# Kernel optimization log

Measured on AMD Instinct MI355X. Metric: run time of the kernel, lower is better.

## Reference

```python
import jax, jax.numpy as jnp
from jax import lax
import numpy as np

B = 128          # batch size
S = 207          # input spatial size implied by outputSpatialSize=[8,8]
N_PTS = 256000
NEG = -1e30      # -inf stand-in for masked max-pooling
# BNReLU channel counts in execution order: 8 resnet blocks x (bn1, bn2), final resnet BN(32), last BN(64)
SIZES = [8,8,8,8,8,16,16,16,16,24,24,24,24,32,32,32,32,64]
OFF = np.cumsum([0] + SIZES)

WSHAPES = dict(conv0=(3,3,1,8),
               c1a=(3,3,8,8), c1b=(3,3,8,8), c2a=(3,3,8,8), c2b=(3,3,8,8),
               c3a=(3,3,8,16), c3b=(3,3,16,16), c3r=(3,3,8,16),
               c4a=(3,3,16,16), c4b=(3,3,16,16),
               c5a=(3,3,16,24), c5b=(3,3,24,24), c5r=(3,3,16,24),
               c6a=(3,3,24,24), c6b=(3,3,24,24),
               c7a=(3,3,24,32), c7b=(3,3,32,32), c7r=(3,3,24,32),
               c8a=(3,3,32,32), c8b=(3,3,32,32),
               conv_last=(5,5,32,64))

def _conv(x, w, stride, padding):
    return lax.conv_general_dilated(x, w, (stride, stride), padding,
                                    dimension_numbers=('NHWC', 'HWIO', 'NHWC'))

def _pool_max(x, win, stride, init):
    return lax.reduce_window(x, init, lax.max, (1, win, win, 1), (1, stride, stride, 1), 'VALID')

def _bnrelu(x, m, g, b):
    # eval-mode BN folded to affine, applied on active sites only (inactive stay exactly 0)
    return m * jax.nn.relu(x * g + b)

def _subconv(x, w, m):
    # submanifold conv == dense conv on zero-filled grid, output restricted to active sites
    return _conv(x, w, 1, 'SAME') * m

def _strided(x, w, m, win, stride):
    # scn.Convolution: output site active iff any active input in its receptive field
    m2 = _pool_max(m, win, stride, 0.0)
    return _conv(x, w, stride, 'VALID') * m2, m2

def _block(x, m, g1, b1, w1, g2, b2, w2, wres, stride):
    # pre-activation basic block from scn.SparseResNet
    h = _bnrelu(x, m, g1, b1)
    if stride == 1:
        h, m2 = _subconv(h, w1, m), m
    else:
        h, m2 = _strided(h, w1, m, 3, 2)
    h = _subconv(_bnrelu(h, m2, g2, b2), w2, m2)
    r = x if wres is None else _strided(x, wres, m, 3, 2)[0]
    return h + r, m2

def _forward(locations, batch_idx, features, bn_gamma, bn_beta, W):
    idx = (batch_idx, locations[:, 0], locations[:, 1], jnp.zeros_like(batch_idx))
    x = jnp.zeros((B, S, S, 1), jnp.float32).at[idx].add(features[:, 0])  # InputLayer (sum dups)
    m = jnp.zeros((B, S, S, 1), jnp.float32).at[idx].set(1.0)             # active-site mask
    g = [bn_gamma[OFF[i]:OFF[i+1]] for i in range(len(SIZES))]
    b = [bn_beta[OFF[i]:OFF[i+1]] for i in range(len(SIZES))]
    x = _subconv(x, W['conv0'], m)                              # 1->8 @ 207x207
    # MaxPooling(pool 3, stride 2) over active sites only
    m2 = _pool_max(m, 3, 2, 0.0)
    x = jnp.where(m2 > 0, _pool_max(jnp.where(m > 0, x, NEG), 3, 2, NEG), 0.0)
    m = m2                                                      # @ 103x103
    blocks = [('c1a', 'c1b', None, 1), ('c2a', 'c2b', None, 1),
              ('c3a', 'c3b', 'c3r', 2), ('c4a', 'c4b', None, 1),
              ('c5a', 'c5b', 'c5r', 2), ('c6a', 'c6b', None, 1),
              ('c7a', 'c7b', 'c7r', 2), ('c8a', 'c8b', None, 1)]
    for i, (k1, k2, kr, st) in enumerate(blocks):
        x, m = _block(x, m, g[2*i], b[2*i], W[k1], g[2*i+1], b[2*i+1], W[k2],
                      None if kr is None else W[kr], st)        # 103->51->25->12
    x = _bnrelu(x, m, g[16], b[16])                             # final resnet BNReLU(32)
    x, m = _strided(x, W['conv_last'], m, 5, 1)                 # 32->64, 12x12 -> 8x8
    x = _bnrelu(x, m, g[17], b[17])
    flat = x.transpose(0, 3, 1, 2).reshape(B, -1)               # SparseToDense + flatten (NCHW order)
    return (flat @ W['w_lin'].T).reshape(B, -1, 1)              # [B, 100, 1]

def setup_inputs():
    key = jax.random.key(0)
    ks = iter(jax.random.split(key, 64))
    inp = {
        'locations': jax.random.randint(next(ks), (N_PTS, 2), 0, S, dtype=jnp.int32),
        'batch_idx': jax.random.randint(next(ks), (N_PTS,), 0, B, dtype=jnp.int32),
        'features': jax.random.normal(next(ks), (N_PTS, 1), jnp.float32),
        'bn_gamma': 1.0 + 0.1 * jax.random.normal(next(ks), (int(OFF[-1]),), jnp.float32),
        'bn_beta': 0.1 * jax.random.normal(next(ks), (int(OFF[-1]),), jnp.float32),
    }
    for name, shp in WSHAPES.items():
        fan_in = int(np.prod(shp[:-1]))
        inp[name] = jax.random.normal(next(ks), shp, jnp.float32) * (2.0 / fan_in) ** 0.5
    inp['w_lin'] = jax.random.normal(next(ks), (100, 64 * 8 * 8), jnp.float32) * (1.0 / 4096.0) ** 0.5
    return inp

def reference(locations, batch_idx, features, bn_gamma, bn_beta, conv0,
              c1a, c1b, c2a, c2b, c3a, c3b, c3r, c4a, c4b, c5a, c5b, c5r,
              c6a, c6b, c7a, c7b, c7r, c8a, c8b, conv_last, w_lin):
    W = dict(conv0=conv0, c1a=c1a, c1b=c1b, c2a=c2a, c2b=c2b, c3a=c3a, c3b=c3b, c3r=c3r,
             c4a=c4a, c4b=c4b, c5a=c5a, c5b=c5b, c5r=c5r, c6a=c6a, c6b=c6b,
             c7a=c7a, c7b=c7b, c7r=c7r, c8a=c8a, c8b=c8b, conv_last=conv_last, w_lin=w_lin)
    return _forward(locations, batch_idx, features, bn_gamma, bn_beta, W)
```

## Files before the change

kernel.cpp:

```cpp
#include <hip/hip_runtime.h>

#define S 207
#define BATCH 128
#define NPTS 256000

static const int OFFS[19] = {0,8,16,24,32,40,56,72,88,104,128,152,176,200,232,264,296,328,392};

__global__ void zero2_kernel(float4* __restrict__ a, float4* __restrict__ b, int n4) {
    int i = blockIdx.x * blockDim.x + threadIdx.x;
    if (i < n4) { a[i] = make_float4(0,0,0,0); b[i] = make_float4(0,0,0,0); }
}

__global__ void zero_kernel(float* __restrict__ p, int n) {
    int i = blockIdx.x * blockDim.x + threadIdx.x;
    if (i < n) p[i] = 0.0f;
}

__global__ void scatter_kernel(const int* __restrict__ loc, const int* __restrict__ bidx,
                               const float* __restrict__ feat,
                               float* __restrict__ xs, float* __restrict__ ms) {
    int t = blockIdx.x * blockDim.x + threadIdx.x;
    if (t >= NPTS) return;
    int b = bidx[t];
    int r = loc[2 * t];
    int c = loc[2 * t + 1];
    int idx = (b * S + r) * S + c;
    atomicAdd(&xs[idx], feat[t]);
    ms[idx] = 1.0f;
}

__global__ __launch_bounds__(256) void conv0_pool_kernel(
    const float* __restrict__ xs, const float* __restrict__ ms,
    const float* __restrict__ w,
    float* __restrict__ x1, float* __restrict__ m1) {
    const int Hout = 103;
    int opix = blockIdx.x * 256 + threadIdx.x;
    int total = BATCH * Hout * Hout;
    if (opix >= total) return;
    int wo = opix % Hout;
    int t = opix / Hout;
    int ho = t % Hout;
    int b  = t / Hout;

    float mv[3][3];
    float mwin = 0.0f;
    #pragma unroll
    for (int pi = 0; pi < 3; ++pi)
        #pragma unroll
        for (int pj = 0; pj < 3; ++pj) {
            float m = ms[(b * S + 2 * ho + pi) * S + 2 * wo + pj];
            mv[pi][pj] = m;
            mwin = fmaxf(mwin, m);
        }
    float* xp = x1 + (size_t)opix * 8;
    if (mwin <= 0.0f) {
        *(float4*)xp = make_float4(0,0,0,0);
        *(float4*)(xp + 4) = make_float4(0,0,0,0);
        m1[opix] = 0.0f;
        return;
    }
    float p[5][5];
    #pragma unroll
    for (int r = 0; r < 5; ++r) {
        int ii = 2 * ho - 1 + r;
        #pragma unroll
        for (int c = 0; c < 5; ++c) {
            int jj = 2 * wo - 1 + c;
            bool ok = ((unsigned)ii < (unsigned)S) && ((unsigned)jj < (unsigned)S);
            p[r][c] = ok ? xs[(b * S + ii) * S + jj] : 0.0f;
        }
    }
    float best[8];
    #pragma unroll
    for (int co = 0; co < 8; ++co) best[co] = -1e30f;
    #pragma unroll
    for (int pi = 0; pi < 3; ++pi)
        #pragma unroll
        for (int pj = 0; pj < 3; ++pj) {
            if (mv[pi][pj] > 0.0f) {
                float acc[8];
                #pragma unroll
                for (int co = 0; co < 8; ++co) acc[co] = 0.0f;
                #pragma unroll
                for (int kh = 0; kh < 3; ++kh)
                    #pragma unroll
                    for (int kw = 0; kw < 3; ++kw) {
                        float x = p[pi + kh][pj + kw];
                        #pragma unroll
                        for (int co = 0; co < 8; ++co)
                            acc[co] = fmaf(x, w[(kh * 3 + kw) * 8 + co], acc[co]);
                    }
                #pragma unroll
                for (int co = 0; co < 8; ++co) best[co] = fmaxf(best[co], acc[co]);
            }
        }
    *(float4*)xp = make_float4(best[0], best[1], best[2], best[3]);
    *(float4*)(xp + 4) = make_float4(best[4], best[5], best[6], best[7]);
    m1[opix] = 1.0f;
}

template <int K, int CIN, int COUT, int COT, bool BN, bool RES>
__global__ __launch_bounds__(256) void fconv_kernel(
    const float* __restrict__ in, const float* __restrict__ w,
    const float* __restrict__ g, const float* __restrict__ bbn,
    const float* __restrict__ mIn, const float* __restrict__ mOut,
    const float* __restrict__ res, float* __restrict__ out,
    int Hin, int Hout, int stride, int pad) {
    const int Win = Hin, Wout = Hout;
    int npix = BATCH * Hout * Wout;
    int opix = blockIdx.x * 256 + threadIdx.x;
    if (opix >= npix) return;
    int co0 = blockIdx.y * COT;
    int wo = opix % Wout;
    int t = opix / Wout;
    int ho = t % Hout;
    int b  = t / Hout;

    float mo = mOut[opix];
    float* op = out + (size_t)opix * COUT + co0;
    if (mo <= 0.0f) {
        #pragma unroll
        for (int j = 0; j < COT; j += 4) {
            float4 r4 = RES ? *(const float4*)(res + (size_t)opix * COUT + co0 + j)
                            : make_float4(0,0,0,0);
            *(float4*)(op + j) = r4;
        }
        return;
    }
    float acc[COT];
    #pragma unroll
    for (int j = 0; j < COT; ++j) acc[j] = 0.0f;

    #pragma unroll
    for (int kh = 0; kh < K; ++kh) {
        int ih = ho * stride + kh - pad;
        if ((unsigned)ih >= (unsigned)Hin) continue;
        #pragma unroll
        for (int kw = 0; kw < K; ++kw) {
            int iw = wo * stride + kw - pad;
            if ((unsigned)iw >= (unsigned)Win) continue;
            int ipix = (b * Hin + ih) * Win + iw;
            float mi = 1.0f;
            if (BN) { mi = mIn[ipix]; if (mi <= 0.0f) continue; }
            const float* ip = in + (size_t)ipix * CIN;
            const float* wp = w + (kh * K + kw) * CIN * COUT + co0;
            #pragma unroll
            for (int ci = 0; ci < CIN; ci += 4) {
                float4 xv = *(const float4*)(ip + ci);
                if (BN) {
                    xv.x = mi * fmaxf(fmaf(xv.x, g[ci],     bbn[ci]),     0.0f);
                    xv.y = mi * fmaxf(fmaf(xv.y, g[ci + 1], bbn[ci + 1]), 0.0f);
                    xv.z = mi * fmaxf(fmaf(xv.z, g[ci + 2], bbn[ci + 2]), 0.0f);
                    xv.w = mi * fmaxf(fmaf(xv.w, g[ci + 3], bbn[ci + 3]), 0.0f);
                }
                #pragma unroll
                for (int j = 0; j < COT; ++j) {
                    acc[j] = fmaf(xv.x, wp[(ci    ) * COUT + j], acc[j]);
                    acc[j] = fmaf(xv.y, wp[(ci + 1) * COUT + j], acc[j]);
                    acc[j] = fmaf(xv.z, wp[(ci + 2) * COUT + j], acc[j]);
                    acc[j] = fmaf(xv.w, wp[(ci + 3) * COUT + j], acc[j]);
                }
            }
        }
    }
    #pragma unroll
    for (int j = 0; j < COT; j += 4) {
        float4 o4;
        o4.x = acc[j] * mo; o4.y = acc[j+1] * mo; o4.z = acc[j+2] * mo; o4.w = acc[j+3] * mo;
        if (RES) {
            float4 r4 = *(const float4*)(res + (size_t)opix * COUT + co0 + j);
            o4.x += r4.x; o4.y += r4.y; o4.z += r4.z; o4.w += r4.w;
        }
        *(float4*)(op + j) = o4;
    }
}

template <int CIN, int COUT, int COT>
__global__ __launch_bounds__(256) void strided_ra_kernel(
    const float* __restrict__ in,
    const float* __restrict__ wR, const float* __restrict__ wA,
    const float* __restrict__ g, const float* __restrict__ bbn,
    const float* __restrict__ mIn, float* __restrict__ mOutBuf,
    float* __restrict__ outR, float* __restrict__ outA,
    int Hin, int Hout) {
    constexpr int NG = COUT / COT;
    int npix = BATCH * Hout * Hout;
    int opix = blockIdx.x * 256 + threadIdx.x;
    if (opix >= npix) return;
    int path = blockIdx.y / NG;
    int co0  = (blockIdx.y % NG) * COT;
    int wo = opix % Hout;
    int t = opix / Hout;
    int ho = t % Hout;
    int b  = t / Hout;

    const float* wsel = path ? wA : wR;
    float acc[COT];
    #pragma unroll
    for (int j = 0; j < COT; ++j) acc[j] = 0.0f;
    float m2 = 0.0f;

    #pragma unroll
    for (int kh = 0; kh < 3; ++kh) {
        int ih = 2 * ho + kh;
        #pragma unroll
        for (int kw = 0; kw < 3; ++kw) {
            int iw = 2 * wo + kw;
            int ipix = (b * Hin + ih) * Hin + iw;
            float mi = mIn[ipix];
            if (mi <= 0.0f) continue;
            m2 = fmaxf(m2, mi);
            const float* ip = in + (size_t)ipix * CIN;
            const float* wp = wsel + (kh * 3 + kw) * CIN * COUT + co0;
            #pragma unroll
            for (int ci = 0; ci < CIN; ci += 4) {
                float4 xv = *(const float4*)(ip + ci);
                if (path) {
                    xv.x = mi * fmaxf(fmaf(xv.x, g[ci],     bbn[ci]),     0.0f);
                    xv.y = mi * fmaxf(fmaf(xv.y, g[ci + 1], bbn[ci + 1]), 0.0f);
                    xv.z = mi * fmaxf(fmaf(xv.z, g[ci + 2], bbn[ci + 2]), 0.0f);
                    xv.w = mi * fmaxf(fmaf(xv.w, g[ci + 3], bbn[ci + 3]), 0.0f);
                }
                #pragma unroll
                for (int j = 0; j < COT; ++j) {
                    acc[j] = fmaf(xv.x, wp[(ci    ) * COUT + j], acc[j]);
                    acc[j] = fmaf(xv.y, wp[(ci + 1) * COUT + j], acc[j]);
                    acc[j] = fmaf(xv.z, wp[(ci + 2) * COUT + j], acc[j]);
                    acc[j] = fmaf(xv.w, wp[(ci + 3) * COUT + j], acc[j]);
                }
            }
        }
    }
    if (blockIdx.y == 0) mOutBuf[opix] = m2;
    float* op = (path ? outA : outR) + (size_t)opix * COUT + co0;
    #pragma unroll
    for (int j = 0; j < COT; j += 4) {
        float4 o4;
        o4.x = acc[j] * m2; o4.y = acc[j+1] * m2; o4.z = acc[j+2] * m2; o4.w = acc[j+3] * m2;
        *(float4*)(op + j) = o4;
    }
}

__global__ void pool_kernel(const float* __restrict__ in, float* __restrict__ out,
                            int Hin, int Win, int Hout, int Wout, int win, int stride) {
    int tid = blockIdx.x * blockDim.x + threadIdx.x;
    int total = BATCH * Hout * Wout;
    if (tid >= total) return;
    int wo = tid % Wout;
    int p = tid / Wout;
    int ho = p % Hout;
    int b  = p / Hout;
    float mx = 0.0f;
    for (int i = 0; i < win; ++i)
        for (int j = 0; j < win; ++j)
            mx = fmaxf(mx, in[(b * Hin + ho * stride + i) * Win + wo * stride + j]);
    out[tid] = mx;
}

__global__ __launch_bounds__(256) void bn_tr_kernel(
    const float* __restrict__ x, const float* __restrict__ m,
    const float* __restrict__ g, const float* __restrict__ bb,
    float* __restrict__ xt) {
    int tid = blockIdx.x * 256 + threadIdx.x;
    if (tid >= BATCH * 4096) return;
    int c = tid & 63, hw = (tid >> 6) & 63, b = tid >> 12;
    float v = m[b * 64 + hw] * fmaxf(fmaf(x[tid], g[c], bb[c]), 0.0f);
    xt[((size_t)b << 12) + c * 64 + hw] = v;
}

__global__ __launch_bounds__(256) void linear_gemm_kernel(
    const float* __restrict__ xt, const float* __restrict__ wl,
    float* __restrict__ out) {
    int o = blockIdx.x;
    int half = threadIdx.x >> 7;
    int b = threadIdx.x & 127;
    int k0 = blockIdx.y * 512 + half * 256;
    const float* xp = xt + ((size_t)b << 12) + k0;
    const float* wp = wl + o * 4096 + k0;
    float acc = 0.0f;
    #pragma unroll 16
    for (int k = 0; k < 256; k += 4) {
        float4 xv = *(const float4*)(xp + k);
        float4 wv = *(const float4*)(wp + k);
        acc = fmaf(xv.x, wv.x, acc); acc = fmaf(xv.y, wv.y, acc);
        acc = fmaf(xv.z, wv.z, acc); acc = fmaf(xv.w, wv.w, acc);
    }
    atomicAdd(&out[b * 100 + o], acc);
}

template <int K, int CIN, int COUT, int COT, bool BN, bool RES>
static inline void fconv(hipStream_t s, const float* in, const float* w,
                         const float* g, const float* bbn,
                         const float* mIn, const float* mOut, const float* res,
                         float* out, int Hin, int Hout, int stride, int pad) {
    int npix = BATCH * Hout * Hout;
    dim3 grid((npix + 255) / 256, COUT / COT);
    fconv_kernel<K, CIN, COUT, COT, BN, RES><<<grid, 256, 0, s>>>(
        in, w, g, bbn, mIn, mOut, res, out, Hin, Hout, stride, pad);
}

template <int CIN, int COUT, int COT>
static inline void strided_ra(hipStream_t s, const float* in, const float* wR, const float* wA,
                              const float* g, const float* bbn, const float* mIn,
                              float* mOutBuf, float* outR, float* outA, int Hin, int Hout) {
    int npix = BATCH * Hout * Hout;
    dim3 grid((npix + 255) / 256, 2 * (COUT / COT));
    strided_ra_kernel<CIN, COUT, COT><<<grid, 256, 0, s>>>(
        in, wR, wA, g, bbn, mIn, mOutBuf, outR, outA, Hin, Hout);
}

extern "C" void kernel_launch(void* const* d_in, const int* in_sizes, int n_in,
                              void* d_out, int out_size, void* d_ws, size_t ws_size,
                              hipStream_t stream) {
    const int*   loc   = (const int*)d_in[0];
    const int*   bidx  = (const int*)d_in[1];
    const float* feat  = (const float*)d_in[2];
    const float* gamma = (const float*)d_in[3];
    const float* beta  = (const float*)d_in[4];
    const float* Wconv0 = (const float*)d_in[5];
    const float* Wc1a = (const float*)d_in[6];
    const float* Wc1b = (const float*)d_in[7];
    const float* Wc2a = (const float*)d_in[8];
    const float* Wc2b = (const float*)d_in[9];
    const float* Wc3a = (const float*)d_in[10];
    const float* Wc3b = (const float*)d_in[11];
    const float* Wc3r = (const float*)d_in[12];
    const float* Wc4a = (const float*)d_in[13];
    const float* Wc4b = (const float*)d_in[14];
    const float* Wc5a = (const float*)d_in[15];
    const float* Wc5b = (const float*)d_in[16];
    const float* Wc5r = (const float*)d_in[17];
    const float* Wc6a = (const float*)d_in[18];
    const float* Wc6b = (const float*)d_in[19];
    const float* Wc7a = (const float*)d_in[20];
    const float* Wc7b = (const float*)d_in[21];
    const float* Wc7r = (const float*)d_in[22];
    const float* Wc8a = (const float*)d_in[23];
    const float* Wc8b = (const float*)d_in[24];
    const float* Wlast = (const float*)d_in[25];
    const float* wlin  = (const float*)d_in[26];

    const size_t SZB = (size_t)BATCH * 103 * 103 * 8;
    const size_t SZM = (size_t)BATCH * 103 * 103;
    float* b0 = (float*)d_ws;
    float* b1 = b0 + SZB;
    float* b2 = b1 + SZB;
    float* m0 = b2 + SZB;
    float* m1 = m0 + SZM;

    const float* G[18];
    const float* Bt[18];
    for (int i = 0; i < 18; ++i) { G[i] = gamma + OFFS[i]; Bt[i] = beta + OFFS[i]; }

    {
        int n = BATCH * S * S;
        zero2_kernel<<<(n / 4 + 255) / 256, 256, 0, stream>>>((float4*)b1, (float4*)b2, n / 4);
        scatter_kernel<<<(NPTS + 255) / 256, 256, 0, stream>>>(loc, bidx, feat, b1, b2);
        int total = BATCH * 103 * 103;
        conv0_pool_kernel<<<(total + 255) / 256, 256, 0, stream>>>(b1, b2, Wconv0, b0, m0);
    }

    fconv<3, 8, 8, 8, true, false>(stream, b0, Wc1a, G[0], Bt[0], m0, m0, nullptr, b1, 103, 103, 1, 1);
    fconv<3, 8, 8, 8, true, true >(stream, b1, Wc1b, G[1], Bt[1], m0, m0, b0,      b2, 103, 103, 1, 1);
    fconv<3, 8, 8, 8, true, false>(stream, b2, Wc2a, G[2], Bt[2], m0, m0, nullptr, b0, 103, 103, 1, 1);
    fconv<3, 8, 8, 8, true, true >(stream, b0, Wc2b, G[3], Bt[3], m0, m0, b2,      b1, 103, 103, 1, 1);
    strided_ra<8, 16, 8>(stream, b1, Wc3r, Wc3a, G[4], Bt[4], m0, m1, b0, b2, 103, 51);
    fconv<3, 16, 16, 8, true, true >(stream, b2, Wc3b, G[5], Bt[5], m1, m1, b0, b1, 51, 51, 1, 1);
    fconv<3, 16, 16, 8, true, false>(stream, b1, Wc4a, G[6], Bt[6], m1, m1, nullptr, b0, 51, 51, 1, 1);
    fconv<3, 16, 16, 8, true, true >(stream, b0, Wc4b, G[7], Bt[7], m1, m1, b1,      b2, 51, 51, 1, 1);
    strided_ra<16, 24, 8>(stream, b2, Wc5r, Wc5a, G[8], Bt[8], m1, m0, b0, b1, 51, 25);
    fconv<3, 24, 24, 8, true, true >(stream, b1, Wc5b, G[9], Bt[9], m0, m0, b0, b2, 25, 25, 1, 1);
    fconv<3, 24, 24, 8, true, false>(stream, b2, Wc6a, G[10], Bt[10], m0, m0, nullptr, b0, 25, 25, 1, 1);
    fconv<3, 24, 24, 8, true, true >(stream, b0, Wc6b, G[11], Bt[11], m0, m0, b2,      b1, 25, 25, 1, 1);
    strided_ra<24, 32, 4>(stream, b1, Wc7r, Wc7a, G[12], Bt[12], m0, m1, b0, b2, 25, 12);
    fconv<3, 32, 32, 4, true, true >(stream, b2, Wc7b, G[13], Bt[13], m1, m1, b0, b1, 12, 12, 1, 1);
    fconv<3, 32, 32, 4, true, false>(stream, b1, Wc8a, G[14], Bt[14], m1, m1, nullptr, b0, 12, 12, 1, 1);
    fconv<3, 32, 32, 4, true, true >(stream, b0, Wc8b, G[15], Bt[15], m1, m1, b1,      b2, 12, 12, 1, 1);
    pool_kernel<<<(BATCH * 64 + 255) / 256, 256, 0, stream>>>(m1, m0, 12, 12, 8, 8, 5, 1);
    fconv<5, 32, 64, 4, true, false>(stream, b2, Wlast, G[16], Bt[16], m1, m0, nullptr, b0, 12, 8, 1, 0);
    bn_tr_kernel<<<(BATCH * 4096 + 255) / 256, 256, 0, stream>>>(b0, m0, G[17], Bt[17], b1);
    zero_kernel<<<(BATCH * 100 + 255) / 256, 256, 0, stream>>>((float*)d_out, BATCH * 100);
    linear_gemm_kernel<<<dim3(100, 8), 256, 0, stream>>>(b1, wlin, (float*)d_out);
}
```

Measured before the change: 907.9 us.

## Fuse first two 8-channel resnet blocks into tiled shared-memory kernel

Adds a resblock kernel that fuses BN-ReLU, two 3x3 submanifold convs and the residual add for one block. It stages a halo tile of the input in shared memory and keeps the intermediate activation on chip, and it is used for the two 103x103 blocks. This removes two full-resolution global round trips per block and two launches, at the cost of recomputing halo pixels. The COT template argument of the strided_ra calls also changes, and buffers are reassigned to fit the new chain.

```diff
diff --git a/kernel.cpp b/kernel.cpp
--- a/kernel.cpp
+++ b/kernel.cpp
@@ -97,6 +97,118 @@
     *(float4*)xp = make_float4(best[0], best[1], best[2], best[3]);
     *(float4*)(xp + 4) = make_float4(best[4], best[5], best[6], best[7]);
     m1[opix] = 1.0f;
+}
+
+template <int C, int TILE, int NTX>
+__global__ __launch_bounds__(256) void resblock_kernel(
+    const float* __restrict__ in, const float* __restrict__ mask,
+    const float* __restrict__ w1, const float* __restrict__ w2,
+    const float* __restrict__ g1, const float* __restrict__ bb1,
+    const float* __restrict__ g2, const float* __restrict__ bb2,
+    float* __restrict__ out, int H) {
+    constexpr int XT = TILE + 4, HT = TILE + 2;
+    constexpr int XA = XT * XT, HA = HT * HT;
+    __shared__ float xs[C][XA];
+    __shared__ float h1[C][HA];
+    __shared__ float msh[XA];
+
+    int tid = threadIdx.x;
+    int bid = blockIdx.x;
+    int b = bid / (NTX * NTX);
+    int t = bid % (NTX * NTX);
+    int r0 = (t / NTX) * TILE, c0 = (t % NTX) * TILE;
+
+    float gr[C], br[C];
+    #pragma unroll
+    for (int c = 0; c < C; ++c) { gr[c] = g1[c]; br[c] = bb1[c]; }
+
+    for (int i = tid; i < XA; i += 256) {
+        int py = i / XT, px = i % XT;
+        int gy = r0 - 2 + py, gx = c0 - 2 + px;
+        bool ok = (unsigned)gy < (unsigned)H && (unsigned)gx < (unsigned)H;
+        float m = 0.0f;
+        if (ok) m = mask[(size_t)(b * H + gy) * H + gx];
+        msh[i] = m;
+        if (m > 0.0f) {
+            const float* ip = in + ((size_t)(b * H + gy) * H + gx) * C;
+            #pragma unroll
+            for (int c = 0; c < C; ++c)
+                xs[c][i] = m * fmaxf(fmaf(ip[c], gr[c], br[c]), 0.0f);
+        } else {
+            #pragma unroll
+            for (int c = 0; c < C; ++c) xs[c][i] = 0.0f;
+        }
+    }
+    #pragma unroll
+    for (int c = 0; c < C; ++c) { gr[c] = g2[c]; br[c] = bb2[c]; }
+    __syncthreads();
+
+    for (int pos = tid; pos < HA; pos += 256) {
+        int py = pos / HT, px = pos % HT;
+        float mc = msh[(py + 1) * XT + px + 1];
+        float acc[C];
+        #pragma unroll
+        for (int co = 0; co < C; ++co) acc[co] = 0.0f;
+        if (mc > 0.0f) {
+            #pragma unroll
+            for (int kh = 0; kh < 3; ++kh)
+                #pragma unroll
+                for (int kw = 0; kw < 3; ++kw) {
+                    int pix = (py + kh) * XT + px + kw;
+                    const float* wp = w1 + (kh * 3 + kw) * C * C;
+                    #pragma unroll
+                    for (int ci = 0; ci < C; ++ci) {
+                        float xv = xs[ci][pix];
+                        #pragma unroll
+                        for (int co = 0; co < C; ++co)
+                            acc[co] = fmaf(xv, wp[ci * C + co], acc[co]);
+                    }
+                }
+        }
+        #pragma unroll
+        for (int co = 0; co < C; ++co)
+            h1[co][pos] = mc * fmaxf(fmaf(acc[co] * mc, gr[co], br[co]), 0.0f);
+    }
+    __syncthreads();
+
+    {
+        int ty = tid / TILE, tx = tid % TILE;
+        int gy = r0 + ty, gx = c0 + tx;
+        if (gy < H && gx < H) {
+            float mo = msh[(ty + 2) * XT + tx + 2];
+            float acc[C];
+            #pragma unroll
+            for (int co = 0; co < C; ++co) acc[co] = 0.0f;
+            if (mo > 0.0f) {
+                #pragma unroll
+                for (int kh = 0; kh < 3; ++kh)
+                    #pragma unroll
+                    for (int kw = 0; kw < 3; ++kw) {
+                        int pix = (ty + kh) * HT + tx + kw;
+                        const float* wp = w2 + (kh * 3 + kw) * C * C;
+                        #pragma unroll
+                        for (int ci = 0; ci < C; ++ci) {
+                            float xv = h1[ci][pix];
+                            #pragma unroll
+                            for (int co = 0; co < C; ++co)
+                                acc[co] = fmaf(xv, wp[ci * C + co], acc[co]);
+                        }
+                    }
+            }
+            const float* rp = in + ((size_t)(b * H + gy) * H + gx) * C;
+            float* op = out + ((size_t)(b * H + gy) * H + gx) * C;
+            #pragma unroll
+            for (int j = 0; j < C; j += 4) {
+                float4 r4 = *(const float4*)(rp + j);
+                float4 o4;
+                o4.x = fmaf(acc[j],     mo, r4.x);
+                o4.y = fmaf(acc[j + 1], mo, r4.y);
+                o4.z = fmaf(acc[j + 2], mo, r4.z);
+                o4.w = fmaf(acc[j + 3], mo, r4.w);
+                *(float4*)(op + j) = o4;
+            }
+        }
+    }
 }
 
 template <int K, int CIN, int COUT, int COT, bool BN, bool RES>
@@ -360,25 +472,25 @@
         conv0_pool_kernel<<<(total + 255) / 256, 256, 0, stream>>>(b1, b2, Wconv0, b0, m0);
     }
 
-    fconv<3, 8, 8, 8, true, false>(stream, b0, Wc1a, G[0], Bt[0], m0, m0, nullptr, b1, 103, 103, 1, 1);
-    fconv<3, 8, 8, 8, true, true >(stream, b1, Wc1b, G[1], Bt[1], m0, m0, b0,      b2, 103, 103, 1, 1);
-    fconv<3, 8, 8, 8, true, false>(stream, b2, Wc2a, G[2], Bt[2], m0, m0, nullptr, b0, 103, 103, 1, 1);
-    fconv<3, 8, 8, 8, true, true >(stream, b0, Wc2b, G[3], Bt[3], m0, m0, b2,      b1, 103, 103, 1, 1);
-    strided_ra<8, 16, 8>(stream, b1, Wc3r, Wc3a, G[4], Bt[4], m0, m1, b0, b2, 103, 51);
-    fconv<3, 16, 16, 8, true, true >(stream, b2, Wc3b, G[5], Bt[5], m1, m1, b0, b1, 51, 51, 1, 1);
-    fconv<3, 16, 16, 8, true, false>(stream, b1, Wc4a, G[6], Bt[6], m1, m1, nullptr, b0, 51, 51, 1, 1);
-    fconv<3, 16, 16, 8, true, true >(stream, b0, Wc4b, G[7], Bt[7], m1, m1, b1,      b2, 51, 51, 1, 1);
-    strided_ra<16, 24, 8>(stream, b2, Wc5r, Wc5a, G[8], Bt[8], m1, m0, b0, b1, 51, 25);
-    fconv<3, 24, 24, 8, true, true >(stream, b1, Wc5b, G[9], Bt[9], m0, m0, b0, b2, 25, 25, 1, 1);
-    fconv<3, 24, 24, 8, true, false>(stream, b2, Wc6a, G[10], Bt[10], m0, m0, nullptr, b0, 25, 25, 1, 1);
-    fconv<3, 24, 24, 8, true, true >(stream, b0, Wc6b, G[11], Bt[11], m0, m0, b2,      b1, 25, 25, 1, 1);
-    strided_ra<24, 32, 4>(stream, b1, Wc7r, Wc7a, G[12], Bt[12], m0, m1, b0, b2, 25, 12);
-    fconv<3, 32, 32, 4, true, true >(stream, b2, Wc7b, G[13], Bt[13], m1, m1, b0, b1, 12, 12, 1, 1);
-    fconv<3, 32, 32, 4, true, false>(stream, b1, Wc8a, G[14], Bt[14], m1, m1, nullptr, b0, 12, 12, 1, 1);
-    fconv<3, 32, 32, 4, true, true >(stream, b0, Wc8b, G[15], Bt[15], m1, m1, b1,      b2, 12, 12, 1, 1);
+    resblock_kernel<8, 16, 7><<<dim3(7 * 7 * BATCH), 256, 0, stream>>>(
+        b0, m0, Wc1a, Wc1b, G[0], Bt[0], G[1], Bt[1], b1, 103);
+    resblock_kernel<8, 16, 7><<<dim3(7 * 7 * BATCH), 256, 0, stream>>>(
+        b1, m0, Wc2a, Wc2b, G[2], Bt[2], G[3], Bt[3], b2, 103);
+    strided_ra<8, 16, 16>(stream, b2, Wc3r, Wc3a, G[4], Bt[4], m0, m1, b0, b1, 103, 51);
+    fconv<3, 16, 16, 8, true, true >(stream, b1, Wc3b, G[5], Bt[5], m1, m1, b0, b2, 51, 51, 1, 1);
+    fconv<3, 16, 16, 8, true, false>(stream, b2, Wc4a, G[6], Bt[6], m1, m1, nullptr, b0, 51, 51, 1, 1);
+    fconv<3, 16, 16, 8, true, true >(stream, b0, Wc4b, G[7], Bt[7], m1, m1, b2,      b1, 51, 51, 1, 1);
+    strided_ra<16, 24, 24>(stream, b1, Wc5r, Wc5a, G[8], Bt[8], m1, m0, b0, b2, 51, 25);
+    fconv<3, 24, 24, 8, true, true >(stream, b2, Wc5b, G[9], Bt[9], m0, m0, b0, b1, 25, 25, 1, 1);
+    fconv<3, 24, 24, 8, true, false>(stream, b1, Wc6a, G[10], Bt[10], m0, m0, nullptr, b0, 25, 25, 1, 1);
+    fconv<3, 24, 24, 8, true, true >(stream, b0, Wc6b, G[11], Bt[11], m0, m0, b1,      b2, 25, 25, 1, 1);
+    strided_ra<24, 32, 8>(stream, b2, Wc7r, Wc7a, G[12], Bt[12], m0, m1, b0, b1, 25, 12);
+    fconv<3, 32, 32, 4, true, true >(stream, b1, Wc7b, G[13], Bt[13], m1, m1, b0, b2, 12, 12, 1, 1);
+    fconv<3, 32, 32, 4, true, false>(stream, b2, Wc8a, G[14], Bt[14], m1, m1, nullptr, b0, 12, 12, 1, 1);
+    fconv<3, 32, 32, 4, true, true >(stream, b0, Wc8b, G[15], Bt[15], m1, m1, b2,      b1, 12, 12, 1, 1);
     pool_kernel<<<(BATCH * 64 + 255) / 256, 256, 0, stream>>>(m1, m0, 12, 12, 8, 8, 5, 1);
-    fconv<5, 32, 64, 4, true, false>(stream, b2, Wlast, G[16], Bt[16], m1, m0, nullptr, b0, 12, 8, 1, 0);
-    bn_tr_kernel<<<(BATCH * 4096 + 255) / 256, 256, 0, stream>>>(b0, m0, G[17], Bt[17], b1);
+    fconv<5, 32, 64, 4, true, false>(stream, b1, Wlast, G[16], Bt[16], m1, m0, nullptr, b0, 12, 8, 1, 0);
+    bn_tr_kernel<<<(BATCH * 4096 + 255) / 256, 256, 0, stream>>>(b0, m0, G[17], Bt[17], b2);
     zero_kernel<<<(BATCH * 100 + 255) / 256, 256, 0, stream>>>((float*)d_out, BATCH * 100);
-    linear_gemm_kernel<<<dim3(100, 8), 256, 0, stream>>>(b1, wlin, (float*)d_out);
-}
+    linear_gemm_kernel<<<dim3(100, 8), 256, 0, stream>>>(b2, wlin, (float*)d_out);
+}
```

After: 802.0 us. 1.13x faster.
